# Performance work log

Measured on AMD Instinct MI355X. Metric: run time of the kernel, lower is better.

Reference implementation:

```python
import jax, jax.numpy as jnp
import numpy as np

TEMPERATURE = 8.0  # sqrt(head_dim=64)

def setup_inputs() -> dict:
    key = jax.random.key(0)
    kq, kk, kv, km = jax.random.split(key, 4)
    B, H, S, D = 2, 16, 2048, 64
    q = jax.random.normal(kq, (B, H, S, D), dtype=jnp.float32)
    k = jax.random.normal(kk, (B, H, S, D), dtype=jnp.float32)
    v = jax.random.normal(kv, (B, H, S, D), dtype=jnp.float32)
    mask = jax.random.randint(km, (B, 1, 1, S), 0, 2, dtype=jnp.int32)
    return {"q": q, "k": k, "v": v, "mask": mask}

def reference(q, k, v, mask):
    # attn = softmax((q/T) @ k^T) with mask fill of -1e9 (dropout p=0 -> no-op)
    attn = jnp.einsum("bhsd,bhtd->bhst", q / TEMPERATURE, k)  # [B,H,S,S]
    attn = jnp.where(mask == 0, jnp.float32(-1e9), attn)
    attn = jax.nn.softmax(attn, axis=-1)
    # output = v^T @ attn @ v  -> [B,H,D,D]
    out = jnp.einsum("bhsd,bhst->bhdt", v, attn)   # v.transpose(2,3) @ attn
    out = jnp.einsum("bhdt,bhtc->bhdc", out, v)     # @ v
    return (out, attn)
```

## Files before the change

### kernel.cpp

```cpp
#include <hip/hip_runtime.h>
#include <math.h>

#define S_LEN 2048
#define D_DIM 64
#define NBH   32
#define TINV  0.125f
#define C2    0.18033688011112042f

typedef float  f32x4   __attribute__((ext_vector_type(4)));
typedef float  f32x16  __attribute__((ext_vector_type(16)));
typedef short  s16x4   __attribute__((ext_vector_type(4)));
typedef short  s16x8   __attribute__((ext_vector_type(8)));
typedef unsigned u32x4 __attribute__((ext_vector_type(4)));
typedef __bf16 bf16x8  __attribute__((ext_vector_type(8)));

__device__ __forceinline__ short bfc(float f) {
  return __builtin_bit_cast(short, (__bf16)f);
}
__device__ __forceinline__ unsigned pk2(float lo, float hi) {
  unsigned r;
  asm("v_cvt_pk_bf16_f32 %0, %1, %2" : "=v"(r) : "v"(lo), "v"(hi));
  return r;
}

__device__ __forceinline__ f32x4 mfma16(s16x8 a, s16x8 b, f32x4 c) {
  return __builtin_amdgcn_mfma_f32_16x16x32_bf16(
      __builtin_bit_cast(bf16x8, a), __builtin_bit_cast(bf16x8, b), c, 0, 0, 0);
}
__device__ __forceinline__ f32x16 mfma32(s16x8 a, s16x8 b, f32x16 c) {
  return __builtin_amdgcn_mfma_f32_32x32x16_bf16(
      __builtin_bit_cast(bf16x8, a), __builtin_bit_cast(bf16x8, b), c, 0, 0, 0);
}

__device__ __forceinline__ short* ldsp(short* base, int row, int byteoff) {
  return (short*)((char*)base + row * 128 + (byteoff ^ ((row & 7) << 4)));
}

#define BAR_LGKM() asm volatile("s_waitcnt lgkmcnt(0)\n\ts_barrier" ::: "memory")

__global__ __launch_bounds__(256) void prep(
    const float* __restrict__ k, const float* __restrict__ v,
    short* __restrict__ kb16, short* __restrict__ vT)
{
  const int bid = blockIdx.x;
  const int t   = bid & 1023;
  const int bh  = t >> 5;
  const int kt  = t & 31;
  const int tid = threadIdx.x;

  if (bid < 1024) {
    const int st  = tid >> 2;
    const int sd0 = (tid & 3) * 16;
    const float* kp = k + ((size_t)bh * S_LEN + kt * 64 + st) * D_DIM + sd0;
    s16x8 o0, o1;
    #pragma unroll
    for (int j = 0; j < 8; ++j) { o0[j] = bfc(kp[j]); o1[j] = bfc(kp[8 + j]); }
    short* dst = kb16 + ((size_t)bh * S_LEN + kt * 64 + st) * D_DIM + sd0;
    *(s16x8*)dst       = o0;
    *(s16x8*)(dst + 8) = o1;
  } else {
    const int vt0 = (tid & 15) * 4;
    const int vd0 = (tid >> 4) * 4;
    const float* vb = v + ((size_t)bh * S_LEN + kt * 64) * D_DIM;
    f32x4 vr[4];
    #pragma unroll
    for (int i = 0; i < 4; ++i)
      vr[i] = *(const f32x4*)(vb + (size_t)(vt0 + i) * D_DIM + vd0);
    #pragma unroll
    for (int j = 0; j < 4; ++j) {
      s16x4 pk;
      pk[0] = bfc(vr[0][j]); pk[1] = bfc(vr[1][j]);
      pk[2] = bfc(vr[2][j]); pk[3] = bfc(vr[3][j]);
      *(s16x4*)(vT + (size_t)(bh * 64 + vd0 + j) * S_LEN + kt * 64 + vt0) = pk;
    }
  }
}

__global__ __launch_bounds__(256, 3) void attn_fwd(
    const float* __restrict__ q, const short* __restrict__ kb16,
    const short* __restrict__ vT, const int* __restrict__ mask,
    float* __restrict__ attn_out, short* __restrict__ OT)
{
  __shared__ short KVd[2][2][64][64];
  __shared__ float rspart[4][32];

  const int bid   = blockIdx.x;
  const int xcd   = bid & 7;
  const int chunk = bid >> 3;
  const int bh    = xcd * 4 + (chunk >> 5);
  const int qt    = chunk & 31;
  const int b     = bh >> 4;

  const int tid  = threadIdx.x;
  const int wave = tid >> 6;
  const int lane = tid & 63;
  const int lr   = lane & 15;
  const int lg   = lane >> 4;
  const int L31  = lane & 31;
  const int hi   = lane >> 5;
  const int Q0   = qt * 64;

  const int qtile = wave & 1;
  const int tt    = wave >> 1;

  const short* kbb  = kb16 + (size_t)bh * S_LEN * D_DIM;
  const short* vtb  = vT   + (size_t)bh * 64 * S_LEN;
  const int*   mrow = mask + b * S_LEN;

  s16x8 aqv[4];
  {
    const float* qp = q + ((size_t)bh * S_LEN + Q0 + qtile * 32 + L31) * D_DIM + hi * 8;
    #pragma unroll
    for (int ks = 0; ks < 4; ++ks) {
      f32x4 x0 = *(const f32x4*)(qp + ks * 16);
      f32x4 x1 = *(const f32x4*)(qp + ks * 16 + 4);
      s16x8 f;
      #pragma unroll
      for (int j = 0; j < 4; ++j) { f[j] = bfc(x0[j]); f[4 + j] = bfc(x1[j]); }
      aqv[ks] = f;
    }
  }

  f32x16 oacc[2];
  #pragma unroll
  for (int dt = 0; dt < 2; ++dt)
    #pragma unroll
    for (int r = 0; r < 16; ++r) oacc[dt][r] = 0.f;
  float rs = 0.f;

  const int st = tid >> 2;
  const int c0 = (tid & 3) * 32;

  s16x8 kr0, kr1, vr0, vr1;
#define LOADT(KT) do { \
    kr0 = *(const s16x8*)(kbb + (size_t)((KT) * 64 + st) * D_DIM + c0 / 2); \
    kr1 = *(const s16x8*)(kbb + (size_t)((KT) * 64 + st) * D_DIM + c0 / 2 + 8); \
    vr0 = *(const s16x8*)(vtb + (size_t)st * S_LEN + (KT) * 64 + c0 / 2); \
    vr1 = *(const s16x8*)(vtb + (size_t)st * S_LEN + (KT) * 64 + c0 / 2 + 8); \
  } while (0)
#define WRITET(KB, VB) do { \
    *(s16x8*)ldsp((KB), st, c0)      = kr0; \
    *(s16x8*)ldsp((KB), st, c0 + 16) = kr1; \
    *(s16x8*)ldsp((VB), st, c0)      = vr0; \
    *(s16x8*)ldsp((VB), st, c0 + 16) = vr1; \
  } while (0)

  LOADT(0);
  WRITET(&KVd[0][0][0][0], &KVd[0][1][0][0]);
  LOADT(1);
  BAR_LGKM();

  for (int kt = 0; kt < 32; ++kt) {
    const int cur = kt & 1;
    short* KBc = &KVd[cur][0][0][0];
    short* VBc = &KVd[cur][1][0][0];

    if (kt + 1 < 32)
      WRITET(&KVd[cur ^ 1][0][0][0], &KVd[cur ^ 1][1][0][0]);
    if (kt + 2 < 32) LOADT(kt + 2);

    const unsigned long long mbits = __ballot(mrow[kt * 64 + lane] != 0);

    f32x16 sacc;
    #pragma unroll
    for (int r = 0; r < 16; ++r) sacc[r] = 0.f;
    #pragma unroll
    for (int ks = 0; ks < 4; ++ks) {
      s16x8 ak = *(const s16x8*)ldsp(KBc, tt * 32 + L31, ks * 32 + hi * 16);
      sacc = mfma32(ak, aqv[ks], sacc);
    }

    const unsigned mloc = (unsigned)(mbits >> (tt * 32 + hi * 4));
    #pragma unroll
    for (int r = 0; r < 16; ++r) {
      float e = __builtin_amdgcn_exp2f(sacc[r] * C2);
      e = ((mloc >> ((r & 3) + 8 * (r >> 2))) & 1u) ? e : 0.f;
      rs += e;
      sacc[r] = e;
    }

    unsigned a0 = pk2(sacc[0], sacc[1]),   b0 = pk2(sacc[4], sacc[5]);
    unsigned a1 = pk2(sacc[2], sacc[3]),   b1 = pk2(sacc[6], sacc[7]);
    unsigned a2 = pk2(sacc[8], sacc[9]),   b2 = pk2(sacc[12], sacc[13]);
    unsigned a3 = pk2(sacc[10], sacc[11]), b3 = pk2(sacc[14], sacc[15]);
    asm volatile("v_permlane32_swap_b32 %0, %1" : "+v"(a0), "+v"(b0));
    asm volatile("v_permlane32_swap_b32 %0, %1" : "+v"(a1), "+v"(b1));
    asm volatile("v_permlane32_swap_b32 %0, %1" : "+v"(a2), "+v"(b2));
    asm volatile("v_permlane32_swap_b32 %0, %1" : "+v"(a3), "+v"(b3));
    const s16x8 pb0 = __builtin_bit_cast(s16x8, (u32x4){a0, a1, b0, b1});
    const s16x8 pb1 = __builtin_bit_cast(s16x8, (u32x4){a2, a3, b2, b3});

    #pragma unroll
    for (int dt = 0; dt < 2; ++dt) {
      s16x8 bv0 = *(const s16x8*)ldsp(VBc, dt * 32 + L31, tt * 64 + hi * 16);
      s16x8 bv1 = *(const s16x8*)ldsp(VBc, dt * 32 + L31, tt * 64 + 32 + hi * 16);
      oacc[dt] = mfma32(bv0, pb0, oacc[dt]);
      oacc[dt] = mfma32(bv1, pb1, oacc[dt]);
    }

    BAR_LGKM();
  }
#undef LOADT
#undef WRITET

  rs += __shfl_xor(rs, 32, 64);

  __syncthreads();
  if (lane < 32) rspart[wave][lane] = rs;
  float* oex = (float*)&KVd[0][0][0][0];
  if (wave >= 2) {
    #pragma unroll
    for (int dt = 0; dt < 2; ++dt)
      #pragma unroll
      for (int r = 0; r < 16; ++r)
        oex[(wave - 2) * 2048 + dt * 1024 + r * 64 + lane] = oacc[dt][r];
  }
  __syncthreads();

  if (wave < 2) {
    const float rsum = rspart[wave][L31] + rspart[wave + 2][L31];
    const float rinvq = 1.0f / rsum;
    #pragma unroll
    for (int dt = 0; dt < 2; ++dt)
      #pragma unroll
      for (int r = 0; r < 16; ++r) {
        const int d = dt * 32 + (r & 3) + 8 * (r >> 2) + 4 * hi;
        float val = (oacc[dt][r] + oex[wave * 2048 + dt * 1024 + r * 64 + lane]) * rinvq;
        OT[(size_t)(bh * 64 + d) * S_LEN + Q0 + wave * 32 + L31] = bfc(val);
      }
  }

  const int qin = (wave & 1) * 16 + lr;
  const float l2r = -__log2f(rspart[wave >> 1][qin] + rspart[(wave >> 1) + 2][qin]);

  __syncthreads();

  s16x8 aq[2];
  {
    const float* qp = q + ((size_t)bh * S_LEN + Q0 + wave * 16 + lr) * D_DIM + lg * 8;
    #pragma unroll
    for (int kk = 0; kk < 2; ++kk) {
      f32x4 x0 = *(const f32x4*)(qp + kk * 32);
      f32x4 x1 = *(const f32x4*)(qp + kk * 32 + 4);
      s16x8 f;
      #pragma unroll
      for (int j = 0; j < 4; ++j) { f[j] = bfc(x0[j]); f[4 + j] = bfc(x1[j]); }
      aq[kk] = f;
    }
  }

  char* stb = (char*)&KVd[0][0][0][0] + wave * 4096;
  float* abase = attn_out + (size_t)bh * S_LEN * S_LEN + (size_t)(Q0 + wave * 16) * S_LEN;
  const int rrow = lane >> 4;
  const int rcol = lane & 15;

  for (int kt = 0; kt < 32; ++kt) {
    const unsigned long long mbits = __ballot(mrow[kt * 64 + lane] != 0);

    #pragma unroll
    for (int n = 0; n < 4; ++n) {
      f32x4 sacc = (f32x4){0.f, 0.f, 0.f, 0.f};
      #pragma unroll
      for (int kk = 0; kk < 2; ++kk) {
        s16x8 bk = *(const s16x8*)(kbb + (size_t)(kt * 64 + n * 16 + lr) * D_DIM +
                                   kk * 32 + lg * 8);
        sacc = mfma16(bk, aq[kk], sacc);
      }
      const unsigned nib = (unsigned)(mbits >> (n * 16 + lg * 4)) & 0xFu;
      f32x4 pv;
      #pragma unroll
      for (int reg = 0; reg < 4; ++reg) {
        float e = __builtin_amdgcn_exp2f(fmaf(sacc[reg], C2, l2r));
        pv[reg] = (nib & (1u << reg)) ? e : 0.f;
      }
      *(f32x4*)(stb + lr * 256 + ((n * 64 + lg * 16) ^ ((lr & 7) << 4))) = pv;
    }

    #pragma unroll
    for (int i = 0; i < 4; ++i) {
      const int row = i * 4 + rrow;
      f32x4 val = *(const f32x4*)(stb + row * 256 + ((rcol * 16) ^ ((row & 7) << 4)));
      __builtin_nontemporal_store(val,
          (f32x4*)(abase + (size_t)row * S_LEN + kt * 64 + rcol * 4));
    }
  }
}

__global__ __launch_bounds__(256) void vo_gemm(
    const short* __restrict__ vT, const short* __restrict__ OT,
    float* __restrict__ out)
{
  const int bh   = blockIdx.x;
  const int tid  = threadIdx.x;
  const int wave = tid >> 6;
  const int lane = tid & 63;
  const int lr   = lane & 15;
  const int lg   = lane >> 4;

  const short* vb = vT + (size_t)(bh * 64) * S_LEN;
  const short* ob = OT + (size_t)(bh * 64) * S_LEN;

  f32x4 acc[4];
  #pragma unroll
  for (int n = 0; n < 4; ++n) acc[n] = (f32x4){0.f, 0.f, 0.f, 0.f};

  for (int s = 0; s < S_LEN; s += 32) {
    s16x8 a = *(const s16x8*)&vb[(size_t)(wave * 16 + lr) * S_LEN + s + lg * 8];
    #pragma unroll
    for (int n = 0; n < 4; ++n) {
      s16x8 bo = *(const s16x8*)&ob[(size_t)(n * 16 + lr) * S_LEN + s + lg * 8];
      acc[n] = mfma16(a, bo, acc[n]);
    }
  }

  #pragma unroll
  for (int n = 0; n < 4; ++n) {
    #pragma unroll
    for (int reg = 0; reg < 4; ++reg) {
      const int d = wave * 16 + lg * 4 + reg;
      const int c = n * 16 + lr;
      out[(size_t)(bh * 64 + d) * 64 + c] = acc[n][reg];
    }
  }
}

extern "C" void kernel_launch(void* const* d_in, const int* in_sizes, int n_in,
                              void* d_out, int out_size, void* d_ws, size_t ws_size,
                              hipStream_t stream) {
  (void)in_sizes; (void)n_in; (void)out_size; (void)ws_size;
  const float* q    = (const float*)d_in[0];
  const float* k    = (const float*)d_in[1];
  const float* v    = (const float*)d_in[2];
  const int*   mask = (const int*)d_in[3];

  float* out  = (float*)d_out;
  float* attn = out + (size_t)NBH * 64 * 64;

  const size_t HS = (size_t)NBH * 64 * S_LEN;
  short* OT   = (short*)d_ws;
  short* vT   = OT + HS;
  short* kb16 = vT + HS;

  prep<<<dim3(2048), dim3(256), 0, stream>>>(k, v, kb16, vT);
  attn_fwd<<<dim3(1024), dim3(256), 0, stream>>>(q, kb16, vT, mask, attn, OT);
  vo_gemm<<<dim3(NBH), dim3(256), 0, stream>>>(vT, OT, out);
}
```

Before: 225.3 us.

## Restructure attention-probability write so each wave stores full contiguous 4KB row segments

After: 237.4 us. +5.4%, slower.

```diff
diff --git a/kernel.cpp b/kernel.cpp
--- a/kernel.cpp
+++ b/kernel.cpp
@@ -230,58 +230,65 @@
       }
   }
 
-  const int qin = (wave & 1) * 16 + lr;
-  const float l2r = -__log2f(rspart[wave >> 1][qin] + rspart[(wave >> 1) + 2][qin]);
-
   __syncthreads();
 
-  s16x8 aq[2];
-  {
-    const float* qp = q + ((size_t)bh * S_LEN + Q0 + wave * 16 + lr) * D_DIM + lg * 8;
-    #pragma unroll
-    for (int kk = 0; kk < 2; ++kk) {
-      f32x4 x0 = *(const f32x4*)(qp + kk * 32);
-      f32x4 x1 = *(const f32x4*)(qp + kk * 32 + 4);
-      s16x8 f;
-      #pragma unroll
-      for (int j = 0; j < 4; ++j) { f[j] = bfc(x0[j]); f[4 + j] = bfc(x1[j]); }
-      aq[kk] = f;
-    }
-  }
-
-  char* stb = (char*)&KVd[0][0][0][0] + wave * 4096;
-  float* abase = attn_out + (size_t)bh * S_LEN * S_LEN + (size_t)(Q0 + wave * 16) * S_LEN;
-  const int rrow = lane >> 4;
-  const int rcol = lane & 15;
-
-  for (int kt = 0; kt < 32; ++kt) {
-    const unsigned long long mbits = __ballot(mrow[kt * 64 + lane] != 0);
-
-    #pragma unroll
-    for (int n = 0; n < 4; ++n) {
-      f32x4 sacc = (f32x4){0.f, 0.f, 0.f, 0.f};
+  float* stg = (float*)&KVd[0][0][0][0];
+
+  for (int rg = 0; rg < 4; ++rg) {
+    s16x8 aq[2];
+    {
+      const float* qp = q + ((size_t)bh * S_LEN + Q0 + rg * 16 + lr) * D_DIM + lg * 8;
       #pragma unroll
       for (int kk = 0; kk < 2; ++kk) {
-        s16x8 bk = *(const s16x8*)(kbb + (size_t)(kt * 64 + n * 16 + lr) * D_DIM +
-                                   kk * 32 + lg * 8);
-        sacc = mfma16(bk, aq[kk], sacc);
+        f32x4 x0 = *(const f32x4*)(qp + kk * 32);
+        f32x4 x1 = *(const f32x4*)(qp + kk * 32 + 4);
+        s16x8 f;
+        #pragma unroll
+        for (int j = 0; j < 4; ++j) { f[j] = bfc(x0[j]); f[4 + j] = bfc(x1[j]); }
+        aq[kk] = f;
       }
-      const unsigned nib = (unsigned)(mbits >> (n * 16 + lg * 4)) & 0xFu;
-      f32x4 pv;
-      #pragma unroll
-      for (int reg = 0; reg < 4; ++reg) {
-        float e = __builtin_amdgcn_exp2f(fmaf(sacc[reg], C2, l2r));
-        pv[reg] = (nib & (1u << reg)) ? e : 0.f;
+    }
+    const int qidx = (rg & 1) * 16 + lr;
+    const float l2r = -__log2f(rspart[rg >> 1][qidx] + rspart[(rg >> 1) + 2][qidx]);
+    float* rowbase = attn_out + (size_t)bh * S_LEN * S_LEN +
+                     (size_t)(Q0 + rg * 16) * S_LEN;
+
+    for (int tg = 0; tg < 4; ++tg) {
+      #pragma unroll
+      for (int sub = 0; sub < 2; ++sub) {
+        const int kt = tg * 8 + wave * 2 + sub;
+        const unsigned long long mbits = __ballot(mrow[kt * 64 + lane] != 0);
+        #pragma unroll
+        for (int n = 0; n < 4; ++n) {
+          f32x4 sacc = (f32x4){0.f, 0.f, 0.f, 0.f};
+          #pragma unroll
+          for (int kk = 0; kk < 2; ++kk) {
+            s16x8 bk = *(const s16x8*)(kbb + (size_t)(kt * 64 + n * 16 + lr) * D_DIM +
+                                       kk * 32 + lg * 8);
+            sacc = mfma16(bk, aq[kk], sacc);
+          }
+          const unsigned nib = (unsigned)(mbits >> (n * 16 + lg * 4)) & 0xFu;
+          f32x4 pv;
+          #pragma unroll
+          for (int reg = 0; reg < 4; ++reg) {
+            float e = __builtin_amdgcn_exp2f(fmaf(sacc[reg], C2, l2r));
+            pv[reg] = (nib & (1u << reg)) ? e : 0.f;
+          }
+          *(f32x4*)((char*)stg + lr * 2048 +
+              ((wave * 512 + sub * 256 + n * 64 + lg * 16) ^ ((lr & 7) << 4))) = pv;
+        }
       }
-      *(f32x4*)(stb + lr * 256 + ((n * 64 + lg * 16) ^ ((lr & 7) << 4))) = pv;
-    }
-
-    #pragma unroll
-    for (int i = 0; i < 4; ++i) {
-      const int row = i * 4 + rrow;
-      f32x4 val = *(const f32x4*)(stb + row * 256 + ((rcol * 16) ^ ((row & 7) << 4)));
-      __builtin_nontemporal_store(val,
-          (f32x4*)(abase + (size_t)row * S_LEN + kt * 64 + rcol * 4));
+      BAR_LGKM();
+
+      #pragma unroll
+      for (int i = 0; i < 8; ++i) {
+        const int row = wave * 4 + (i >> 1);
+        f32x4 val = *(const f32x4*)((char*)stg + row * 2048 +
+            ((((i & 1) << 10) + lane * 16) ^ ((row & 7) << 4)));
+        __builtin_nontemporal_store(val,
+            (f32x4*)(rowbase + (size_t)row * S_LEN + tg * 512 + (i & 1) * 256 + lane * 4));
+      }
+      BAR_LGKM();
     }
   }
 }
```
